# Kernel tuning notes

Hardware: AMD Instinct MI355X
Metric: run time of the kernel (lower is better)

## Reference

```python
import jax, jax.numpy as jnp
import numpy as np

THRESHOLD = 0.9
DECAY = 0.6


def setup_inputs() -> dict:
    key = jax.random.key(0)
    k1, k2, k3 = jax.random.split(key, 3)
    T, B, I, H, O = 100, 256, 784, 1024, 10
    # binary-ish spike input (rand fill, thresholded to emulate Poisson spikes)
    x = (jax.random.uniform(k1, (T, B, I)) < 0.3).astype(jnp.float32)
    W1 = 0.01 * jax.random.normal(k2, (I, H), dtype=jnp.float32)
    W2 = 0.01 * jax.random.normal(k3, (H, O), dtype=jnp.float32)
    return {"input_spikes_time": x, "W1": W1, "W2": W2}


def reference(input_spikes_time, W1, W2):
    T, B, _ = input_spikes_time.shape
    H = W1.shape[1]
    O = W2.shape[1]
    dt = input_spikes_time.dtype

    def lif(mem, current):
        # mem = mem*decay + I; spike if mem >= threshold; soft reset
        mem = mem * DECAY + current
        spikes = (mem >= THRESHOLD).astype(dt)
        mem = mem - spikes * THRESHOLD
        return mem, spikes

    def step(carry, x_t):
        mem1, mem2 = carry
        hidden_u = x_t @ W1                 # [B, H]
        mem1, hidden_spikes = lif(mem1, hidden_u)
        output_u = hidden_spikes @ W2       # [B, O]
        mem2, output_spikes = lif(mem2, output_u)
        return (mem1, mem2), (hidden_spikes, output_spikes)

    init = (jnp.zeros((B, H), dt), jnp.zeros((B, O), dt))
    _, (hidden_all, output_all) = jax.lax.scan(step, init, input_spikes_time)
    return hidden_all, output_all
```

## Files before the change

### kernel.cpp

```cpp
#include <hip/hip_runtime.h>
#include <hip/hip_bf16.h>

#define T_STEPS 100
#define BATCH   256
#define IN_DIM  784
#define HID_DIM 1024
#define OUT_DIM 10
#define M_ROWS  (T_STEPS * BATCH)
#define KPAD    800
#define DECAY   0.6f
#define THRESH  0.9f

typedef __attribute__((ext_vector_type(8))) short bf16x8;
typedef __attribute__((ext_vector_type(4))) float f32x4;

#define PACK8(dstp, v0, v1)                                                                        \
    {                                                                                              \
        unsigned int p0 = __builtin_amdgcn_perm(__builtin_bit_cast(unsigned int, (v0).y),          \
                                                __builtin_bit_cast(unsigned int, (v0).x), 0x07060302u); \
        unsigned int p1 = __builtin_amdgcn_perm(__builtin_bit_cast(unsigned int, (v0).w),          \
                                                __builtin_bit_cast(unsigned int, (v0).z), 0x07060302u); \
        unsigned int p2 = __builtin_amdgcn_perm(__builtin_bit_cast(unsigned int, (v1).y),          \
                                                __builtin_bit_cast(unsigned int, (v1).x), 0x07060302u); \
        unsigned int p3 = __builtin_amdgcn_perm(__builtin_bit_cast(unsigned int, (v1).w),          \
                                                __builtin_bit_cast(unsigned int, (v1).z), 0x07060302u); \
        *(uint4*)(dstp) = make_uint4(p0, p1, p2, p3);                                              \
    }

__global__ __launch_bounds__(256) void w1_split_T(const float* __restrict__ W1,
                                                  unsigned short* __restrict__ Th,
                                                  unsigned short* __restrict__ Tl) {
    __shared__ unsigned short lh[32][33];
    __shared__ unsigned short ll[32][33];
    const int nb = blockIdx.x * 32;
    const int kb = blockIdx.y * 32;
    const int t  = threadIdx.x;
    const int ln = t & 31, lk = t >> 5;
    #pragma unroll
    for (int i = 0; i < 4; ++i) {
        const int k = kb + lk + i * 8;
        const float w = (k < IN_DIM) ? W1[(size_t)k * HID_DIM + nb + ln] : 0.f;
        __hip_bfloat16 h = __float2bfloat16(w);
        float hf = __bfloat162float(h);
        __hip_bfloat16 l = __float2bfloat16(w - hf);
        lh[lk + i * 8][ln] = __builtin_bit_cast(unsigned short, h);
        ll[lk + i * 8][ln] = __builtin_bit_cast(unsigned short, l);
    }
    __syncthreads();
    const int o_n = t >> 3;
    const int o_k = (t & 7) * 4;
    ushort4 vh, vl;
    vh.x = lh[o_k + 0][o_n]; vh.y = lh[o_k + 1][o_n];
    vh.z = lh[o_k + 2][o_n]; vh.w = lh[o_k + 3][o_n];
    vl.x = ll[o_k + 0][o_n]; vl.y = ll[o_k + 1][o_n];
    vl.z = ll[o_k + 2][o_n]; vl.w = ll[o_k + 3][o_n];
    *(ushort4*)&Th[(size_t)(nb + o_n) * KPAD + kb + o_k] = vh;
    *(ushort4*)&Tl[(size_t)(nb + o_n) * KPAD + kb + o_k] = vl;
}

__global__ __launch_bounds__(256, 3) void gemm1_mfma(const float* __restrict__ X,
                                                     const unsigned short* __restrict__ Th,
                                                     const unsigned short* __restrict__ Tl,
                                                     float* __restrict__ C) {
    __shared__ unsigned short As[128 * 32];
    __shared__ unsigned short Bhs[128 * 32];
    __shared__ unsigned short Bls[128 * 32];

    const int tid = threadIdx.x;
    const int bid = blockIdx.x;
    const int xcd = bid & 7;
    const int j_  = bid >> 3;
    const int m0  = (xcd * 25 + (j_ >> 3)) * 128;
    const int n0  = (j_ & 7) * 128;

    const int lane = tid & 63, wv = tid >> 6;
    const int wm   = (wv & 1) * 64, wn = (wv >> 1) * 64;
    const int ml   = lane & 15, quad = lane >> 4;

    const int sr = tid >> 2;
    const int sc = tid & 3;
    const int f0 = (sr >> 1) & 3;
    const int w0 = sr * 32 + ((sc ^ f0) * 8);
    const int w1 = (sr + 64) * 32 + ((sc ^ f0) * 8);

    const float*          Xa = X  + (size_t)(m0 + sr)      * IN_DIM + sc * 8;
    const float*          Xb = X  + (size_t)(m0 + sr + 64) * IN_DIM + sc * 8;
    const unsigned short* Ha = Th + (size_t)(n0 + sr)      * KPAD   + sc * 8;
    const unsigned short* Hb = Th + (size_t)(n0 + sr + 64) * KPAD   + sc * 8;
    const unsigned short* La = Tl + (size_t)(n0 + sr)      * KPAD   + sc * 8;
    const unsigned short* Lb = Tl + (size_t)(n0 + sr + 64) * KPAD   + sc * 8;

    f32x4 acc[4][4];
    #pragma unroll
    for (int i = 0; i < 4; ++i)
        #pragma unroll
        for (int j = 0; j < 4; ++j)
            acc[i][j] = (f32x4){0.f, 0.f, 0.f, 0.f};

    float4 xa0 = *(const float4*)&Xa[0], xa1 = *(const float4*)&Xa[4];
    float4 xb0 = *(const float4*)&Xb[0], xb1 = *(const float4*)&Xb[4];
    uint4  vh0 = *(const uint4*)&Ha[0],  vh1 = *(const uint4*)&Hb[0];
    uint4  vl0 = *(const uint4*)&La[0],  vl1 = *(const uint4*)&Lb[0];
    PACK8(&As[w0], xa0, xa1);
    PACK8(&As[w1], xb0, xb1);
    *(uint4*)&Bhs[w0] = vh0;  *(uint4*)&Bhs[w1] = vh1;
    *(uint4*)&Bls[w0] = vl0;  *(uint4*)&Bls[w1] = vl1;
    __syncthreads();

    for (int it = 0; it < KPAD / 32; ++it) {
        bf16x8 af[4], bh[4], bl[4];
        #pragma unroll
        for (int i = 0; i < 4; ++i) {
            const int m = wm + i * 16 + ml;
            af[i] = *(const bf16x8*)&As[m * 32 + ((quad ^ ((m >> 1) & 3)) * 8)];
        }
        #pragma unroll
        for (int j = 0; j < 4; ++j) {
            const int n   = wn + j * 16 + ml;
            const int idx = n * 32 + ((quad ^ ((n >> 1) & 3)) * 8);
            bh[j] = *(const bf16x8*)&Bhs[idx];
            bl[j] = *(const bf16x8*)&Bls[idx];
        }

        const bool have_next = (it + 1 < KPAD / 32);
        if (have_next) {
            const int kt = (it + 1) * 32;
            const int c0 = kt + sc * 8;
            const bool v0 = (c0 < IN_DIM), v1 = (c0 + 4 < IN_DIM);
            xa0 = v0 ? *(const float4*)&Xa[kt]     : make_float4(0.f, 0.f, 0.f, 0.f);
            xa1 = v1 ? *(const float4*)&Xa[kt + 4] : make_float4(0.f, 0.f, 0.f, 0.f);
            xb0 = v0 ? *(const float4*)&Xb[kt]     : make_float4(0.f, 0.f, 0.f, 0.f);
            xb1 = v1 ? *(const float4*)&Xb[kt + 4] : make_float4(0.f, 0.f, 0.f, 0.f);
            vh0 = *(const uint4*)&Ha[kt];  vh1 = *(const uint4*)&Hb[kt];
            vl0 = *(const uint4*)&La[kt];  vl1 = *(const uint4*)&Lb[kt];
        }

        #pragma unroll
        for (int i = 0; i < 4; ++i)
            #pragma unroll
            for (int j = 0; j < 4; ++j) {
                acc[i][j] = __builtin_amdgcn_mfma_f32_16x16x32_bf16(af[i], bh[j], acc[i][j], 0, 0, 0);
                acc[i][j] = __builtin_amdgcn_mfma_f32_16x16x32_bf16(af[i], bl[j], acc[i][j], 0, 0, 0);
            }

        __syncthreads();
        if (have_next) {
            PACK8(&As[w0], xa0, xa1);
            PACK8(&As[w1], xb0, xb1);
            *(uint4*)&Bhs[w0] = vh0;  *(uint4*)&Bhs[w1] = vh1;
            *(uint4*)&Bls[w0] = vl0;  *(uint4*)&Bls[w1] = vl1;
            __syncthreads();
        }
    }

    #pragma unroll
    for (int i = 0; i < 4; ++i)
        #pragma unroll
        for (int j = 0; j < 4; ++j) {
            const int row = m0 + wm + i * 16 + quad * 4;
            const int col = n0 + wn + j * 16 + ml;
            #pragma unroll
            for (int r = 0; r < 4; ++r)
                C[(size_t)(row + r) * HID_DIM + col] = acc[i][j][r];
        }
}

__global__ __launch_bounds__(256) void lif1_fused(float* __restrict__ hid,
                                                  const float* __restrict__ W2,
                                                  float* __restrict__ outu) {
    const int idx = blockIdx.x * blockDim.x + threadIdx.x;
    float4* h4 = (float4*)hid;
    const int stride4 = (BATCH * HID_DIM) / 4;
    const int b  = (idx * 4) >> 10;
    const int h0 = (idx * 4) & 1023;

    float4 mem = make_float4(0.f, 0.f, 0.f, 0.f);
    float4 u[4];
    #pragma unroll
    for (int c = 0; c < 4; ++c) u[c] = h4[c * stride4 + idx];

    for (int t = 0; t < T_STEPS; t += 4) {
        float4 nu[4];
        if (t + 4 < T_STEPS) {
            #pragma unroll
            for (int c = 0; c < 4; ++c) nu[c] = h4[(t + 4 + c) * stride4 + idx];
        }
        #pragma unroll
        for (int c = 0; c < 4; ++c) {
            float4 uu = u[c];
            float4 s;
            mem.x = mem.x * DECAY + uu.x; s.x = (mem.x >= THRESH) ? 1.f : 0.f; mem.x -= s.x * THRESH;
            mem.y = mem.y * DECAY + uu.y; s.y = (mem.y >= THRESH) ? 1.f : 0.f; mem.y -= s.y * THRESH;
            mem.z = mem.z * DECAY + uu.z; s.z = (mem.z >= THRESH) ? 1.f : 0.f; mem.z -= s.z * THRESH;
            mem.w = mem.w * DECAY + uu.w; s.w = (mem.w >= THRESH) ? 1.f : 0.f; mem.w -= s.w * THRESH;
            h4[(t + c) * stride4 + idx] = s;
            if (s.x + s.y + s.z + s.w > 0.f) {
                float* od = outu + (size_t)(t + c) * (BATCH * OUT_DIM) + b * OUT_DIM;
                #pragma unroll
                for (int e = 0; e < 4; ++e) {
                    const float sv = (&s.x)[e];
                    if (sv != 0.f) {
                        const float* w = W2 + (size_t)(h0 + e) * OUT_DIM;
                        #pragma unroll
                        for (int o = 0; o < OUT_DIM; ++o) atomicAdd(&od[o], w[o]);
                    }
                }
            }
        }
        #pragma unroll
        for (int c = 0; c < 4; ++c) u[c] = nu[c];
    }
}

__global__ __launch_bounds__(256) void lif2(float* __restrict__ outp) {
    const int n = blockIdx.x * blockDim.x + threadIdx.x;
    const int stride = BATCH * OUT_DIM;
    if (n >= stride) return;
    float mem = 0.f;
    float u[4];
    #pragma unroll
    for (int c = 0; c < 4; ++c) u[c] = outp[c * stride + n];
    for (int t = 0; t < T_STEPS; t += 4) {
        float nu[4];
        if (t + 4 < T_STEPS) {
            #pragma unroll
            for (int c = 0; c < 4; ++c) nu[c] = outp[(t + 4 + c) * stride + n];
        }
        #pragma unroll
        for (int c = 0; c < 4; ++c) {
            mem = mem * DECAY + u[c];
            float s = (mem >= THRESH) ? 1.f : 0.f;
            mem -= s * THRESH;
            outp[(t + c) * stride + n] = s;
        }
        #pragma unroll
        for (int c = 0; c < 4; ++c) u[c] = nu[c];
    }
}

extern "C" void kernel_launch(void* const* d_in, const int* in_sizes, int n_in,
                              void* d_out, int out_size, void* d_ws, size_t ws_size,
                              hipStream_t stream) {
    const float* x  = (const float*)d_in[0];
    const float* W1 = (const float*)d_in[1];
    const float* W2 = (const float*)d_in[2];
    float* out  = (float*)d_out;
    float* hid  = out;
    float* outu = out + (size_t)M_ROWS * HID_DIM;

    unsigned short* Th = (unsigned short*)d_ws;
    unsigned short* Tl = Th + (size_t)HID_DIM * KPAD;

    dim3 gt(HID_DIM / 32, KPAD / 32);
    w1_split_T<<<gt, 256, 0, stream>>>(W1, Th, Tl);

    hipMemsetAsync(outu, 0, (size_t)M_ROWS * OUT_DIM * sizeof(float), stream);

    gemm1_mfma<<<1600, 256, 0, stream>>>(x, Th, Tl, hid);

    lif1_fused<<<(BATCH * HID_DIM / 4) / 256, 256, 0, stream>>>(hid, W2, outu);

    lif2<<<(BATCH * OUT_DIM + 255) / 256, 256, 0, stream>>>(outu);
}
```

Before: 302.8 us.

## Pre-convert X to bf16 and triple-buffer GEMM with direct global-to-LDS loads

Adds a prep kernel that converts the spike input X to padded bf16 in workspace, splits W1 and zeroes the output buffer, replacing the separate transpose kernel and memset. The GEMM now streams A, Bh and Bl tiles into a three-stage LDS ring with global_load_lds, using vmcnt waits, a single barrier per iteration and raised priority around the MFMAs. The LIF kernel is changed to process two hidden units per thread, doubling the thread count. The new GEMM path depends on the workspace being large enough and otherwise falls back to the old kernel. The extra bf16 copy of X adds a pass over the input in exchange for halving the bytes the GEMM reads.

```diff
diff --git a/kernel.cpp b/kernel.cpp
--- a/kernel.cpp
+++ b/kernel.cpp
@@ -8,6 +8,8 @@
 #define OUT_DIM 10
 #define M_ROWS  (T_STEPS * BATCH)
 #define KPAD    800
+#define NT      25
+#define STG     12288
 #define DECAY   0.6f
 #define THRESH  0.9f
 
@@ -27,14 +29,18 @@
         *(uint4*)(dstp) = make_uint4(p0, p1, p2, p3);                                              \
     }
 
-__global__ __launch_bounds__(256) void w1_split_T(const float* __restrict__ W1,
-                                                  unsigned short* __restrict__ Th,
-                                                  unsigned short* __restrict__ Tl) {
-    __shared__ unsigned short lh[32][33];
-    __shared__ unsigned short ll[32][33];
-    const int nb = blockIdx.x * 32;
-    const int kb = blockIdx.y * 32;
-    const int t  = threadIdx.x;
+#define GLL(g, l)                                                                                  \
+    __builtin_amdgcn_global_load_lds((const __attribute__((address_space(1))) void*)(g),           \
+                                     (__attribute__((address_space(3))) void*)(l), 16, 0, 0)
+
+__device__ __forceinline__ void w1_split_body(const float* __restrict__ W1,
+                                              unsigned short* __restrict__ Th,
+                                              unsigned short* __restrict__ Tl,
+                                              int b2, int t,
+                                              unsigned short lh[32][33],
+                                              unsigned short ll[32][33]) {
+    const int nb = (b2 & 31) * 32;
+    const int kb = (b2 >> 5) * 32;
     const int ln = t & 31, lk = t >> 5;
     #pragma unroll
     for (int i = 0; i < 4; ++i) {
@@ -58,13 +64,58 @@
     *(ushort4*)&Tl[(size_t)(nb + o_n) * KPAD + kb + o_k] = vl;
 }
 
-__global__ __launch_bounds__(256, 3) void gemm1_mfma(const float* __restrict__ X,
+__global__ __launch_bounds__(256) void prep(const float* __restrict__ X,
+                                            const float* __restrict__ W1,
+                                            unsigned short* __restrict__ Xb,
+                                            unsigned short* __restrict__ Th,
+                                            unsigned short* __restrict__ Tl,
+                                            float* __restrict__ outu) {
+    __shared__ unsigned short lh[32][33];
+    __shared__ unsigned short ll[32][33];
+    const int bid = blockIdx.x;
+    const int t   = threadIdx.x;
+
+    if (bid < 10000) {
+        const int gid = bid * 256 + t;
+        const int r   = gid / 100;
+        const int c   = gid - r * 100;
+        unsigned short* dst = Xb + (size_t)r * KPAD + c * 8;
+        if (c < 98) {
+            const float* s = X + (size_t)r * IN_DIM + c * 8;
+            float4 v0 = *(const float4*)s, v1 = *(const float4*)(s + 4);
+            PACK8(dst, v0, v1);
+        } else {
+            *(uint4*)dst = make_uint4(0u, 0u, 0u, 0u);
+        }
+    } else if (bid < 10800) {
+        w1_split_body(W1, Th, Tl, bid - 10000, t, lh, ll);
+    } else {
+        float4* p = (float4*)outu;
+        p[(bid - 10800) * 256 + t] = make_float4(0.f, 0.f, 0.f, 0.f);
+    }
+}
+
+__global__ __launch_bounds__(256) void prep_small(const float* __restrict__ W1,
+                                                  unsigned short* __restrict__ Th,
+                                                  unsigned short* __restrict__ Tl,
+                                                  float* __restrict__ outu) {
+    __shared__ unsigned short lh[32][33];
+    __shared__ unsigned short ll[32][33];
+    const int bid = blockIdx.x;
+    const int t   = threadIdx.x;
+    if (bid < 800) {
+        w1_split_body(W1, Th, Tl, bid, t, lh, ll);
+    } else {
+        float4* p = (float4*)outu;
+        p[(bid - 800) * 256 + t] = make_float4(0.f, 0.f, 0.f, 0.f);
+    }
+}
+
+__global__ __launch_bounds__(256, 2) void gemm1_pipe(const unsigned short* __restrict__ Xb,
                                                      const unsigned short* __restrict__ Th,
                                                      const unsigned short* __restrict__ Tl,
                                                      float* __restrict__ C) {
-    __shared__ unsigned short As[128 * 32];
-    __shared__ unsigned short Bhs[128 * 32];
-    __shared__ unsigned short Bls[128 * 32];
+    __shared__ unsigned short smem[3 * STG];
 
     const int tid = threadIdx.x;
     const int bid = blockIdx.x;
@@ -77,6 +128,119 @@
     const int wm   = (wv & 1) * 64, wn = (wv >> 1) * 64;
     const int ml   = lane & 15, quad = lane >> 4;
 
+    const int row  = tid >> 2;
+    const int slot = tid & 3;
+    const int sOff = (slot ^ ((row >> 1) & 3)) * 8;
+
+    const unsigned short* gA0 = Xb + (size_t)(m0 + row)      * KPAD + sOff;
+    const unsigned short* gA1 = Xb + (size_t)(m0 + row + 64) * KPAD + sOff;
+    const unsigned short* gH0 = Th + (size_t)(n0 + row)      * KPAD + sOff;
+    const unsigned short* gH1 = Th + (size_t)(n0 + row + 64) * KPAD + sOff;
+    const unsigned short* gL0 = Tl + (size_t)(n0 + row)      * KPAD + sOff;
+    const unsigned short* gL1 = Tl + (size_t)(n0 + row + 64) * KPAD + sOff;
+
+#define STAGE(bf, it)                                                     \
+    {                                                                     \
+        unsigned short* b_ = smem + (bf) * STG;                           \
+        const int k_ = (it) * 32;                                         \
+        GLL(gA0 + k_, b_ + tid * 8);                                      \
+        GLL(gA1 + k_, b_ + 2048 + tid * 8);                               \
+        GLL(gH0 + k_, b_ + 4096 + tid * 8);                               \
+        GLL(gH1 + k_, b_ + 6144 + tid * 8);                               \
+        GLL(gL0 + k_, b_ + 8192 + tid * 8);                               \
+        GLL(gL1 + k_, b_ + 10240 + tid * 8);                              \
+    }
+
+    f32x4 acc[4][4];
+    #pragma unroll
+    for (int i = 0; i < 4; ++i)
+        #pragma unroll
+        for (int j = 0; j < 4; ++j)
+            acc[i][j] = (f32x4){0.f, 0.f, 0.f, 0.f};
+
+    int offA[4], offB[4];
+    #pragma unroll
+    for (int i = 0; i < 4; ++i) {
+        const int m = wm + i * 16 + ml;
+        offA[i] = m * 32 + ((quad ^ ((m >> 1) & 3)) * 8);
+    }
+    #pragma unroll
+    for (int j = 0; j < 4; ++j) {
+        const int n = wn + j * 16 + ml;
+        offB[j] = n * 32 + ((quad ^ ((n >> 1) & 3)) * 8);
+    }
+
+    STAGE(0, 0);
+    STAGE(1, 1);
+
+    int buf = 0;
+    for (int it = 0; it < NT; ++it) {
+        if (it < NT - 1) asm volatile("s_waitcnt vmcnt(6)" ::: "memory");
+        else             asm volatile("s_waitcnt vmcnt(0)" ::: "memory");
+        __builtin_amdgcn_s_barrier();
+        asm volatile("" ::: "memory");
+
+        if (it + 2 < NT) {
+            int nb = buf + 2; if (nb >= 3) nb -= 3;
+            STAGE(nb, it + 2);
+        }
+
+        const unsigned short* base = smem + buf * STG;
+        bf16x8 af[4], bh[4], bl[4];
+        #pragma unroll
+        for (int i = 0; i < 4; ++i)
+            af[i] = *(const bf16x8*)&base[offA[i]];
+        #pragma unroll
+        for (int j = 0; j < 4; ++j) {
+            bh[j] = *(const bf16x8*)&base[4096 + offB[j]];
+            bl[j] = *(const bf16x8*)&base[8192 + offB[j]];
+        }
+
+        __builtin_amdgcn_s_setprio(1);
+        #pragma unroll
+        for (int i = 0; i < 4; ++i)
+            #pragma unroll
+            for (int j = 0; j < 4; ++j) {
+                acc[i][j] = __builtin_amdgcn_mfma_f32_16x16x32_bf16(af[i], bh[j], acc[i][j], 0, 0, 0);
+                acc[i][j] = __builtin_amdgcn_mfma_f32_16x16x32_bf16(af[i], bl[j], acc[i][j], 0, 0, 0);
+            }
+        __builtin_amdgcn_s_setprio(0);
+
+        buf = (buf == 2) ? 0 : buf + 1;
+    }
+#undef STAGE
+
+    #pragma unroll
+    for (int i = 0; i < 4; ++i)
+        #pragma unroll
+        for (int j = 0; j < 4; ++j) {
+            const int r0 = m0 + wm + i * 16 + quad * 4;
+            const int c0 = n0 + wn + j * 16 + ml;
+            #pragma unroll
+            for (int r = 0; r < 4; ++r)
+                C[(size_t)(r0 + r) * HID_DIM + c0] = acc[i][j][r];
+        }
+}
+
+__global__ __launch_bounds__(256, 3) void gemm1_fallback(const float* __restrict__ X,
+                                                         const unsigned short* __restrict__ Th,
+                                                         const unsigned short* __restrict__ Tl,
+                                                         float* __restrict__ C) {
+    __shared__ unsigned short As[128 * 32];
+    __shared__ unsigned short Bhs[128 * 32];
+    __shared__ unsigned short Bls[128 * 32];
+
+    const int tid = threadIdx.x;
+    const int bid = blockIdx.x;
+    const int xcd = bid & 7;
+    const int j_  = bid >> 3;
+    const int m0  = (xcd * 25 + (j_ >> 3)) * 128;
+    const int n0  = (j_ & 7) * 128;
+
+    const int lane = tid & 63, wv = tid >> 6;
+    const int wm   = (wv & 1) * 64, wn = (wv >> 1) * 64;
+    const int ml   = lane & 15, quad = lane >> 4;
+
     const int sr = tid >> 2;
     const int sc = tid & 3;
     const int f0 = (sr >> 1) & 3;
@@ -84,7 +248,7 @@
     const int w1 = (sr + 64) * 32 + ((sc ^ f0) * 8);
 
     const float*          Xa = X  + (size_t)(m0 + sr)      * IN_DIM + sc * 8;
-    const float*          Xb = X  + (size_t)(m0 + sr + 64) * IN_DIM + sc * 8;
+    const float*          Xc = X  + (size_t)(m0 + sr + 64) * IN_DIM + sc * 8;
     const unsigned short* Ha = Th + (size_t)(n0 + sr)      * KPAD   + sc * 8;
     const unsigned short* Hb = Th + (size_t)(n0 + sr + 64) * KPAD   + sc * 8;
     const unsigned short* La = Tl + (size_t)(n0 + sr)      * KPAD   + sc * 8;
@@ -98,7 +262,7 @@
             acc[i][j] = (f32x4){0.f, 0.f, 0.f, 0.f};
 
     float4 xa0 = *(const float4*)&Xa[0], xa1 = *(const float4*)&Xa[4];
-    float4 xb0 = *(const float4*)&Xb[0], xb1 = *(const float4*)&Xb[4];
+    float4 xb0 = *(const float4*)&Xc[0], xb1 = *(const float4*)&Xc[4];
     uint4  vh0 = *(const uint4*)&Ha[0],  vh1 = *(const uint4*)&Hb[0];
     uint4  vl0 = *(const uint4*)&La[0],  vl1 = *(const uint4*)&Lb[0];
     PACK8(&As[w0], xa0, xa1);
@@ -107,7 +271,7 @@
     *(uint4*)&Bls[w0] = vl0;  *(uint4*)&Bls[w1] = vl1;
     __syncthreads();
 
-    for (int it = 0; it < KPAD / 32; ++it) {
+    for (int it = 0; it < NT; ++it) {
         bf16x8 af[4], bh[4], bl[4];
         #pragma unroll
         for (int i = 0; i < 4; ++i) {
@@ -122,15 +286,15 @@
             bl[j] = *(const bf16x8*)&Bls[idx];
         }
 
-        const bool have_next = (it + 1 < KPAD / 32);
+        const bool have_next = (it + 1 < NT);
         if (have_next) {
             const int kt = (it + 1) * 32;
             const int c0 = kt + sc * 8;
             const bool v0 = (c0 < IN_DIM), v1 = (c0 + 4 < IN_DIM);
             xa0 = v0 ? *(const float4*)&Xa[kt]     : make_float4(0.f, 0.f, 0.f, 0.f);
             xa1 = v1 ? *(const float4*)&Xa[kt + 4] : make_float4(0.f, 0.f, 0.f, 0.f);
-            xb0 = v0 ? *(const float4*)&Xb[kt]     : make_float4(0.f, 0.f, 0.f, 0.f);
-            xb1 = v1 ? *(const float4*)&Xb[kt + 4] : make_float4(0.f, 0.f, 0.f, 0.f);
+            xb0 = v0 ? *(const float4*)&Xc[kt]     : make_float4(0.f, 0.f, 0.f, 0.f);
+            xb1 = v1 ? *(const float4*)&Xc[kt + 4] : make_float4(0.f, 0.f, 0.f, 0.f);
             vh0 = *(const uint4*)&Ha[kt];  vh1 = *(const uint4*)&Hb[kt];
             vl0 = *(const uint4*)&La[kt];  vl1 = *(const uint4*)&Lb[kt];
         }
@@ -157,11 +321,11 @@
     for (int i = 0; i < 4; ++i)
         #pragma unroll
         for (int j = 0; j < 4; ++j) {
-            const int row = m0 + wm + i * 16 + quad * 4;
-            const int col = n0 + wn + j * 16 + ml;
+            const int r0 = m0 + wm + i * 16 + quad * 4;
+            const int c0 = n0 + wn + j * 16 + ml;
             #pragma unroll
             for (int r = 0; r < 4; ++r)
-                C[(size_t)(row + r) * HID_DIM + col] = acc[i][j][r];
+                C[(size_t)(r0 + r) * HID_DIM + c0] = acc[i][j][r];
         }
 }
 
@@ -169,35 +333,33 @@
                                                   const float* __restrict__ W2,
                                                   float* __restrict__ outu) {
     const int idx = blockIdx.x * blockDim.x + threadIdx.x;
-    float4* h4 = (float4*)hid;
-    const int stride4 = (BATCH * HID_DIM) / 4;
-    const int b  = (idx * 4) >> 10;
-    const int h0 = (idx * 4) & 1023;
-
-    float4 mem = make_float4(0.f, 0.f, 0.f, 0.f);
-    float4 u[4];
-    #pragma unroll
-    for (int c = 0; c < 4; ++c) u[c] = h4[c * stride4 + idx];
+    float2* h2 = (float2*)hid;
+    const int stride2 = (BATCH * HID_DIM) / 2;
+    const int b  = idx >> 9;
+    const int h0 = (idx * 2) & 1023;
+
+    float2 mem = make_float2(0.f, 0.f);
+    float2 u[4];
+    #pragma unroll
+    for (int c = 0; c < 4; ++c) u[c] = h2[c * stride2 + idx];
 
     for (int t = 0; t < T_STEPS; t += 4) {
-        float4 nu[4];
+        float2 nu[4];
         if (t + 4 < T_STEPS) {
             #pragma unroll
-            for (int c = 0; c < 4; ++c) nu[c] = h4[(t + 4 + c) * stride4 + idx];
+            for (int c = 0; c < 4; ++c) nu[c] = h2[(t + 4 + c) * stride2 + idx];
         }
         #pragma unroll
         for (int c = 0; c < 4; ++c) {
-            float4 uu = u[c];
-            float4 s;
+            float2 uu = u[c];
+            float2 s;
             mem.x = mem.x * DECAY + uu.x; s.x = (mem.x >= THRESH) ? 1.f : 0.f; mem.x -= s.x * THRESH;
             mem.y = mem.y * DECAY + uu.y; s.y = (mem.y >= THRESH) ? 1.f : 0.f; mem.y -= s.y * THRESH;
-            mem.z = mem.z * DECAY + uu.z; s.z = (mem.z >= THRESH) ? 1.f : 0.f; mem.z -= s.z * THRESH;
-            mem.w = mem.w * DECAY + uu.w; s.w = (mem.w >= THRESH) ? 1.f : 0.f; mem.w -= s.w * THRESH;
-            h4[(t + c) * stride4 + idx] = s;
-            if (s.x + s.y + s.z + s.w > 0.f) {
+            h2[(t + c) * stride2 + idx] = s;
+            if (s.x + s.y > 0.f) {
                 float* od = outu + (size_t)(t + c) * (BATCH * OUT_DIM) + b * OUT_DIM;
                 #pragma unroll
-                for (int e = 0; e < 4; ++e) {
+                for (int e = 0; e < 2; ++e) {
                     const float sv = (&s.x)[e];
                     if (sv != 0.f) {
                         const float* w = W2 + (size_t)(h0 + e) * OUT_DIM;
@@ -250,15 +412,21 @@
 
     unsigned short* Th = (unsigned short*)d_ws;
     unsigned short* Tl = Th + (size_t)HID_DIM * KPAD;
-
-    dim3 gt(HID_DIM / 32, KPAD / 32);
-    w1_split_T<<<gt, 256, 0, stream>>>(W1, Th, Tl);
-
-    hipMemsetAsync(outu, 0, (size_t)M_ROWS * OUT_DIM * sizeof(float), stream);
-
-    gemm1_mfma<<<1600, 256, 0, stream>>>(x, Th, Tl, hid);
-
-    lif1_fused<<<(BATCH * HID_DIM / 4) / 256, 256, 0, stream>>>(hid, W2, outu);
+    unsigned short* Xb = Tl + (size_t)HID_DIM * KPAD;
+
+    const size_t ws_needed_big =
+        (size_t)2 * HID_DIM * KPAD * sizeof(unsigned short) +
+        (size_t)M_ROWS * KPAD * sizeof(unsigned short);
+
+    if (ws_size >= ws_needed_big) {
+        prep<<<11050, 256, 0, stream>>>(x, W1, Xb, Th, Tl, outu);
+        gemm1_pipe<<<1600, 256, 0, stream>>>(Xb, Th, Tl, hid);
+    } else {
+        prep_small<<<1050, 256, 0, stream>>>(W1, Th, Tl, outu);
+        gemm1_fallback<<<1600, 256, 0, stream>>>(x, Th, Tl, hid);
+    }
+
+    lif1_fused<<<(BATCH * HID_DIM / 2) / 256, 256, 0, stream>>>(hid, W2, outu);
 
     lif2<<<(BATCH * OUT_DIM + 255) / 256, 256, 0, stream>>>(outu);
 }
```

After: 278.4 us. 1.09x faster.
